# Optimization experiments

Hardware: AMD Instinct MI355X
Metric: run time of the kernel (lower is better)

The kernel has to match this reference:

```python
import jax, jax.numpy as jnp
import numpy as np

MARGIN = 0.3
BIG = 9999999.0


def setup_inputs() -> dict:
    key = jax.random.key(0)
    k1, k2, k3 = jax.random.split(key, 3)
    N, D, D2, NUM_IDS = 8192, 1024, 512, 512
    emb = jax.random.normal(k1, (N, D), dtype=jnp.float32)
    clot_feats_s = jax.random.normal(k2, (N, D2), dtype=jnp.float32)
    label = jax.random.randint(k3, (N,), 0, NUM_IDS, dtype=jnp.int64)
    return {"emb": emb, "label": label, "clot_feats_s": clot_feats_s}


def _margin_ranking_loss(x1, x2, y, margin):
    # torch MarginRankingLoss: mean(max(0, -y*(x1-x2)+margin))
    return jnp.mean(jnp.maximum(0.0, -y * (x1 - x2) + margin))


def reference(emb, label, clot_feats_s):
    N = emb.shape[0]
    # euclidean_dist(emb, emb): [N,N]
    sq = jnp.sum(emb * emb, axis=1)
    dist = sq[:, None] + sq[None, :] - 2.0 * (emb @ emb.T)
    dist = jnp.sqrt(jnp.clip(dist, 1e-12, None))
    # cosine similarity of clot_feats_s with itself: [N,N]
    nrm = jnp.sqrt(jnp.sum(clot_feats_s * clot_feats_s, axis=1))
    cos = (clot_feats_s @ clot_feats_s.T) / (nrm[:, None] * nrm[None, :])
    # same-identity mask
    sim = (label[:, None] == label[None, :]).astype(dist.dtype)
    # batch-hard: top-2 positives (largest masked distance), hardest negative (smallest)
    pos_vals, pos_idx = jax.lax.top_k(dist - BIG * (1.0 - sim), 2)
    dist_ap1, dist_ap2 = pos_vals[:, 0], pos_vals[:, 1]
    neg_mat = dist + BIG * sim
    hard_n_idx = jnp.argmin(neg_mat, axis=1)
    dist_an = jnp.min(neg_mat, axis=1)
    rows = jnp.arange(N)
    # per-row gathers into cosine-sim matrix (detached in original)
    alpha1 = jax.lax.stop_gradient(cos[rows, pos_idx[:, 0]])
    alpha2 = jax.lax.stop_gradient(cos[rows, pos_idx[:, 1]])
    # (alphan gathered in original but unused in the loss)
    y11 = jnp.where(alpha1 < alpha2, -1.0, 1.0)
    y11_m = jnp.where(alpha1 == alpha2, 0.0, 1.0)
    loss11 = _margin_ranking_loss(
        dist_ap2 * y11_m,
        dist_ap1 * y11_m + MARGIN * (alpha1 - alpha2 - y11),
        y11, MARGIN)
    dist_ap1_m = dist_ap1 + MARGIN * (alpha1 - 1.0)
    loss13 = _margin_ranking_loss(dist_an, dist_ap1_m, 1.0, MARGIN)
    loss = 0.1 * loss11 + loss13
    prec = jnp.mean((dist_an > dist_ap1_m).astype(jnp.float32))
    return loss, prec
```

## Files before the change

kernel.cpp:

```cpp
#include <hip/hip_runtime.h>
#include <stdint.h>

#define NR 8192
#define DE 1024
#define DC 512
#define BIGF 9999999.0f
#define MARG 0.3f
#define NEGI -3.0e38f
#define POSI 3.0e38f

typedef __attribute__((ext_vector_type(8))) short bf16x8;
typedef __attribute__((ext_vector_type(4))) float f32x4;

typedef __attribute__((address_space(3))) unsigned int lds_u32;
typedef const __attribute__((address_space(1))) unsigned int glb_u32;

static __device__ __forceinline__ void ld_g2l16(const void* g, void* l) {
    __builtin_amdgcn_global_load_lds((glb_u32*)g, (lds_u32*)l, 16, 0, 0);
}

static __device__ __forceinline__ unsigned short f2bf(float x) {
    unsigned u = __float_as_uint(x);
    unsigned r = u + 0x7FFFu + ((u >> 16) & 1u);
    return (unsigned short)(r >> 16);
}

static __device__ __forceinline__ float b2f(short u) {
    return __uint_as_float(((unsigned)(unsigned short)u) << 16);
}

__global__ __launch_bounds__(256) void k_prep_emb(const float* __restrict__ emb,
                                                  const int* __restrict__ label,
                                                  short* __restrict__ embb,
                                                  float* __restrict__ sq,
                                                  int* __restrict__ cnt) {
    int row = blockIdx.x, tid = threadIdx.x;
    float4 v = ((const float4*)(emb + (size_t)row * DE))[tid];
    float s = v.x * v.x + v.y * v.y + v.z * v.z + v.w * v.w;
    ushort4 b;
    b.x = f2bf(v.x); b.y = f2bf(v.y); b.z = f2bf(v.z); b.w = f2bf(v.w);
    *(ushort4*)&embb[(size_t)row * DE + tid * 4] = b;
    for (int m = 1; m < 64; m <<= 1) s += __shfl_xor(s, m);
    __shared__ float red[4];
    if ((tid & 63) == 0) red[tid >> 6] = s;
    __syncthreads();
    if (tid == 0) {
        sq[row] = red[0] + red[1] + red[2] + red[3];
        atomicAdd(&cnt[label[row]], 1);
    }
}

__global__ __launch_bounds__(256) void k_fill(const int* __restrict__ cnt,
                                              const int* __restrict__ label,
                                              int* __restrict__ clsOff,
                                              int* __restrict__ fill,
                                              int* __restrict__ list) {
    __shared__ int s[512];
    int t = threadIdx.x;
    s[t] = cnt[t];
    s[t + 256] = cnt[t + 256];
    __syncthreads();
    for (int d = 1; d < 512; d <<= 1) {
        int v0 = (t >= d) ? s[t - d] : 0;
        int v1 = s[t + 256 - d];
        __syncthreads();
        s[t] += v0;
        s[t + 256] += v1;
        __syncthreads();
    }
    if (blockIdx.x == 0) {
        clsOff[t] = s[t] - cnt[t];
        clsOff[t + 256] = s[t + 256] - cnt[t + 256];
    }
    int i = blockIdx.x * 256 + t;
    int l = label[i];
    int p = atomicAdd(&fill[l], 1);
    list[s[l] - cnt[l] + p] = i;
}

__global__ __launch_bounds__(256, 3) void k_main(const short* __restrict__ embb,
                                                 const float* __restrict__ sq,
                                                 const int* __restrict__ label,
                                                 unsigned* __restrict__ mnA) {
    const int b = blockIdx.x;
    int r = (int)((129.0f - sqrtf(16641.0f - 8.0f * (float)b)) * 0.5f);
    if (r < 0) r = 0;
    if (r > 63) r = 63;
    while (r > 0 && 64 * r - (r * (r - 1)) / 2 > b) --r;
    while (64 * (r + 1) - ((r + 1) * r) / 2 <= b) ++r;
    const int c = r + (b - (64 * r - (r * (r - 1)) / 2));
    const int i0 = r * 128, j0 = c * 128;

    __shared__ __align__(16) short As[128 * 64];
    __shared__ __align__(16) short Bs[128 * 64];

    const int tid = threadIdx.x;
    const int lane = tid & 63;
    const int w = tid >> 6;
    const int wr = w >> 1, wc = w & 1;
    const int q = lane >> 4, l15 = lane & 15;

    const int g = (tid & 7) ^ ((tid >> 3) & 7);
    const short* gA = embb + (size_t)(i0 + (tid >> 3)) * DE + g * 8;
    const short* gB = embb + (size_t)(j0 + (tid >> 3)) * DE + g * 8;

    const int swz = l15 & 7;

    auto stage = [&](int koff) {
#pragma unroll
        for (int n = 0; n < 4; ++n) {
            ld_g2l16(gA + (size_t)n * 32 * DE + koff, &As[n * 2048 + tid * 8]);
            ld_g2l16(gB + (size_t)n * 32 * DE + koff, &Bs[n * 2048 + tid * 8]);
        }
    };

    stage(0);

    f32x4 acc[4][4];
#pragma unroll
    for (int mi = 0; mi < 4; ++mi)
#pragma unroll
        for (int ni = 0; ni < 4; ++ni) acc[mi][ni] = (f32x4){0.f, 0.f, 0.f, 0.f};

    for (int ks = 0; ks < 16; ++ks) {
        __syncthreads();
        bf16x8 af[2][4], bfr[2][4];
#pragma unroll
        for (int kk = 0; kk < 2; ++kk) {
            const int kc = ((kk * 4 + q) ^ swz) * 8;
#pragma unroll
            for (int mi = 0; mi < 4; ++mi)
                af[kk][mi] = *(const bf16x8*)&As[(wr * 64 + mi * 16 + l15) * 64 + kc];
#pragma unroll
            for (int ni = 0; ni < 4; ++ni)
                bfr[kk][ni] = *(const bf16x8*)&Bs[(wc * 64 + ni * 16 + l15) * 64 + kc];
        }
#pragma unroll
        for (int kk = 0; kk < 2; ++kk)
#pragma unroll
            for (int mi = 0; mi < 4; ++mi)
#pragma unroll
                for (int ni = 0; ni < 4; ++ni)
                    acc[mi][ni] = __builtin_amdgcn_mfma_f32_16x16x32_bf16(af[kk][mi], bfr[kk][ni], acc[mi][ni], 0, 0, 0);
        __syncthreads();
        if (ks < 15) stage((ks + 1) * 64);
    }

    const int rb = i0 + wr * 64, cb = j0 + wc * 64;
    float sqj[4]; int lbj[4]; float cmn[4];
#pragma unroll
    for (int ni = 0; ni < 4; ++ni) {
        int cg = cb + ni * 16 + l15;
        sqj[ni] = sq[cg]; lbj[ni] = label[cg]; cmn[ni] = POSI;
    }
#pragma unroll
    for (int mi = 0; mi < 4; ++mi) {
        float rm[4] = {POSI, POSI, POSI, POSI};
        float sqi[4]; int lbi[4];
#pragma unroll
        for (int rr = 0; rr < 4; ++rr) {
            int rg = rb + mi * 16 + q * 4 + rr;
            sqi[rr] = sq[rg]; lbi[rr] = label[rg];
        }
#pragma unroll
        for (int ni = 0; ni < 4; ++ni)
#pragma unroll
            for (int rr = 0; rr < 4; ++rr) {
                float d2 = fmaf(-2.0f, acc[mi][ni][rr], sqi[rr] + sqj[ni]);
                d2 = fmaxf(d2, 1e-12f);
                float dn = (lbi[rr] == lbj[ni]) ? POSI : d2;
                rm[rr] = fminf(rm[rr], dn);
                cmn[ni] = fminf(cmn[ni], dn);
            }
#pragma unroll
        for (int rr = 0; rr < 4; ++rr) {
            float v = rm[rr];
            v = fminf(v, __shfl_xor(v, 1));
            v = fminf(v, __shfl_xor(v, 2));
            v = fminf(v, __shfl_xor(v, 4));
            v = fminf(v, __shfl_xor(v, 8));
            if (l15 == 0) atomicMin(&mnA[rb + mi * 16 + q * 4 + rr], __float_as_uint(v));
        }
    }
#pragma unroll
    for (int ni = 0; ni < 4; ++ni) {
        float v = cmn[ni];
        v = fminf(v, __shfl_xor(v, 16));
        v = fminf(v, __shfl_xor(v, 32));
        if (q == 0) atomicMin(&mnA[cb + ni * 16 + l15], __float_as_uint(v));
    }
}

__global__ __launch_bounds__(256) void k_pos(const short* __restrict__ embb,
                                             const float* __restrict__ sq,
                                             const float* __restrict__ clot,
                                             const int* __restrict__ label,
                                             const int* __restrict__ cnt,
                                             const int* __restrict__ clsOff,
                                             const int* __restrict__ clsList,
                                             const unsigned* __restrict__ mnA,
                                             float* __restrict__ ap1, float* __restrict__ ap2,
                                             float* __restrict__ an,
                                             float* __restrict__ alpha1, float* __restrict__ alpha2) {
    int wid = threadIdx.x >> 6, lane = threadIdx.x & 63;
    int row = blockIdx.x * 4 + wid;
    int lb = label[row];
    int cc = cnt[lb], off = clsOff[lb];
    float sqiv = sq[row];

    const bf16x8* rp = (const bf16x8*)(embb + (size_t)row * DE + lane * 16);
    bf16x8 ra = rp[0], rb = rp[1];
    float rf[16];
#pragma unroll
    for (int t = 0; t < 8; ++t) { rf[t] = b2f(ra[t]); rf[8 + t] = b2f(rb[t]); }

    float v1 = NEGI, v2 = NEGI;
    int i1 = 0, i2 = 0;

    auto upd = [&](float d2, int j) {
        bool t1 = (d2 > v1) || (d2 == v1 && j < i1);
        bool t2 = (d2 > v2) || (d2 == v2 && j < i2);
        v2 = t1 ? v1 : (t2 ? d2 : v2);
        i2 = t1 ? i1 : (t2 ? j : i2);
        v1 = t1 ? d2 : v1;
        i1 = t1 ? j : i1;
    };

    int m = 0;
    for (; m + 2 <= cc; m += 2) {
        int ja = clsList[off + m], jb = clsList[off + m + 1];
        const bf16x8* pa = (const bf16x8*)(embb + (size_t)ja * DE + lane * 16);
        const bf16x8* pb = (const bf16x8*)(embb + (size_t)jb * DE + lane * 16);
        bf16x8 a0 = pa[0], a1v = pa[1];
        bf16x8 b0 = pb[0], b1v = pb[1];
        float sa = 0.f, sb = 0.f;
#pragma unroll
        for (int t = 0; t < 8; ++t) { sa = fmaf(rf[t], b2f(a0[t]), sa); sb = fmaf(rf[t], b2f(b0[t]), sb); }
#pragma unroll
        for (int t = 0; t < 8; ++t) { sa = fmaf(rf[8 + t], b2f(a1v[t]), sa); sb = fmaf(rf[8 + t], b2f(b1v[t]), sb); }
        for (int mm = 1; mm < 64; mm <<= 1) { sa += __shfl_xor(sa, mm); sb += __shfl_xor(sb, mm); }
        float d2a = fmaxf(fmaf(-2.0f, sa, sqiv + sq[ja]), 1e-12f);
        float d2b = fmaxf(fmaf(-2.0f, sb, sqiv + sq[jb]), 1e-12f);
        if (ja == row) d2a = 1e-12f;
        if (jb == row) d2b = 1e-12f;
        upd(d2a, ja);
        upd(d2b, jb);
    }
    if (m < cc) {
        int j = clsList[off + m];
        float d2;
        if (j == row) {
            d2 = 1e-12f;
        } else {
            const bf16x8* jp = (const bf16x8*)(embb + (size_t)j * DE + lane * 16);
            bf16x8 ja0 = jp[0], ja1 = jp[1];
            float s = 0.f;
#pragma unroll
            for (int t = 0; t < 8; ++t) s = fmaf(rf[t], b2f(ja0[t]), s);
#pragma unroll
            for (int t = 0; t < 8; ++t) s = fmaf(rf[8 + t], b2f(ja1[t]), s);
            for (int mm = 1; mm < 64; mm <<= 1) s += __shfl_xor(s, mm);
            d2 = fmaxf(fmaf(-2.0f, s, sqiv + sq[j]), 1e-12f);
        }
        upd(d2, j);
    }

    float a1 = sqrtf(v1);
    int j1 = i1;
    float a2v; int j2;
    if (cc >= 2) {
        a2v = sqrtf(v2);
        j2 = i2;
    } else {
        float kv = NEGI; int ki = 0;
        for (int cr = lane; cr < NR; cr += 64) {
            if (label[cr] == lb) continue;
            float s = 0.f;
            const short* crow = embb + (size_t)cr * DE;
            const short* rrow = embb + (size_t)row * DE;
            for (int t = 0; t < DE; ++t) s = fmaf(b2f(rrow[t]), b2f(crow[t]), s);
            float d2c = fmaxf(fmaf(-2.0f, s, sqiv + sq[cr]), 1e-12f);
            bool tk = (d2c > kv) || (d2c == kv && cr < ki);
            kv = tk ? d2c : kv; ki = tk ? cr : ki;
        }
        for (int mm = 1; mm < 64; mm <<= 1) {
            float ov = __shfl_xor(kv, mm); int oi = __shfl_xor(ki, mm);
            bool tk = (ov > kv) || (ov == kv && oi < ki);
            kv = tk ? ov : kv; ki = tk ? oi : ki;
        }
        a2v = sqrtf(kv) - BIGF;
        j2 = ki;
    }

    const float4* c4 = (const float4*)clot;
    float s1 = 0.f, s2 = 0.f, n0 = 0.f, n1 = 0.f, n2 = 0.f;
    for (int t = lane; t < DC / 4; t += 64) {
        float4 a = c4[(size_t)row * (DC / 4) + t];
        float4 b1 = c4[(size_t)j1 * (DC / 4) + t];
        float4 b2 = c4[(size_t)j2 * (DC / 4) + t];
        s1 += a.x * b1.x + a.y * b1.y + a.z * b1.z + a.w * b1.w;
        s2 += a.x * b2.x + a.y * b2.y + a.z * b2.z + a.w * b2.w;
        n0 += a.x * a.x + a.y * a.y + a.z * a.z + a.w * a.w;
        n1 += b1.x * b1.x + b1.y * b1.y + b1.z * b1.z + b1.w * b1.w;
        n2 += b2.x * b2.x + b2.y * b2.y + b2.z * b2.z + b2.w * b2.w;
    }
    for (int mm = 1; mm < 64; mm <<= 1) {
        s1 += __shfl_xor(s1, mm); s2 += __shfl_xor(s2, mm);
        n0 += __shfl_xor(n0, mm); n1 += __shfl_xor(n1, mm); n2 += __shfl_xor(n2, mm);
    }
    if (lane == 0) {
        ap1[row] = a1; ap2[row] = a2v;
        an[row] = sqrtf(__uint_as_float(mnA[row]));
        alpha1[row] = s1 / (sqrtf(n0) * sqrtf(n1));
        alpha2[row] = s2 / (sqrtf(n0) * sqrtf(n2));
    }
}

__global__ __launch_bounds__(256) void k_final(const float* __restrict__ ap1, const float* __restrict__ ap2,
                                               const float* __restrict__ an,
                                               const float* __restrict__ alpha1, const float* __restrict__ alpha2,
                                               float* __restrict__ out) {
    int tid = threadIdx.x;
    float sl11 = 0.f, sl13 = 0.f, sp = 0.f;
    for (int row = tid; row < NR; row += 256) {
        float a1 = alpha1[row], a2 = alpha2[row];
        float dap1 = ap1[row], dap2 = ap2[row], dan = an[row];
        float y = (a1 < a2) ? -1.f : 1.f;
        float ym = (a1 == a2) ? 0.f : 1.f;
        float x1 = dap2 * ym;
        float x2 = dap1 * ym + MARG * (a1 - a2 - y);
        sl11 += fmaxf(0.f, -y * (x1 - x2) + MARG);
        float ap1m = dap1 + MARG * (a1 - 1.f);
        sl13 += fmaxf(0.f, -(dan - ap1m) + MARG);
        sp += (dan > ap1m) ? 1.f : 0.f;
    }
    for (int m = 1; m < 64; m <<= 1) {
        sl11 += __shfl_xor(sl11, m);
        sl13 += __shfl_xor(sl13, m);
        sp += __shfl_xor(sp, m);
    }
    __shared__ float r11[4], r13[4], rp[4];
    if ((tid & 63) == 0) { r11[tid >> 6] = sl11; r13[tid >> 6] = sl13; rp[tid >> 6] = sp; }
    __syncthreads();
    if (tid == 0) {
        float t11 = r11[0] + r11[1] + r11[2] + r11[3];
        float t13 = r13[0] + r13[1] + r13[2] + r13[3];
        float tp = rp[0] + rp[1] + rp[2] + rp[3];
        out[0] = 0.1f * (t11 / (float)NR) + t13 / (float)NR;
        out[1] = tp / (float)NR;
    }
}

extern "C" void kernel_launch(void* const* d_in, const int* in_sizes, int n_in,
                              void* d_out, int out_size, void* d_ws, size_t ws_size,
                              hipStream_t stream) {
    const float* emb = (const float*)d_in[0];
    const int* label = (const int*)d_in[1];
    const float* clot = (const float*)d_in[2];
    float* out = (float*)d_out;

    char* ws = (char*)d_ws;
    size_t off = 0;
    auto alloc = [&](size_t bytes) -> char* {
        char* p = ws + off;
        off = (off + bytes + 255) & ~(size_t)255;
        return p;
    };
    short*    embb = (short*)alloc((size_t)NR * DE * 2);
    float*    sq   = (float*)alloc(NR * 4);
    int*      cnt  = (int*)alloc(512 * 4);
    int*      fill = (int*)alloc(512 * 4);
    int*      cOff = (int*)alloc(512 * 4);
    int*      list = (int*)alloc(NR * 4);
    unsigned* mnA  = (unsigned*)alloc((size_t)NR * 4);
    float*    ap1  = (float*)alloc(NR * 4);
    float*    ap2  = (float*)alloc(NR * 4);
    float*    an   = (float*)alloc(NR * 4);
    float*    al1  = (float*)alloc(NR * 4);
    float*    al2  = (float*)alloc(NR * 4);

    hipMemsetAsync(cnt, 0, 2 * 512 * 4, stream);
    hipMemsetAsync(mnA, 0xFF, (size_t)NR * 4, stream);

    k_prep_emb<<<dim3(NR), dim3(256), 0, stream>>>(emb, label, embb, sq, cnt);
    k_fill<<<dim3(NR / 256), dim3(256), 0, stream>>>(cnt, label, cOff, fill, list);
    k_main<<<dim3(2080), dim3(256), 0, stream>>>(embb, sq, label, mnA);
    k_pos<<<dim3(NR / 4), dim3(256), 0, stream>>>(embb, sq, clot, label, cnt, cOff, list,
                                                  mnA, ap1, ap2, an, al1, al2);
    k_final<<<dim3(1), dim3(256), 0, stream>>>(ap1, ap2, an, al1, al2, out);
}
```

Baseline: 232.7 us.

## Split each row's positive search across four waves and fold mnA init into prep

k_pos now gives each row a whole 256-thread block instead of one wave. The four waves split the same-class candidate list and merge their top-2 results through shared memory. The rare fallback scan is also spread over all 256 threads. Separately, the memset of the min-distance buffer is replaced by a store in k_prep_emb, which removes one memset launch. This adds parallelism to a latency-bound per-row loop, at the cost of more blocks, a block barrier, and three idle waves during the cosine stage.

```diff
diff --git a/kernel.cpp b/kernel.cpp
--- a/kernel.cpp
+++ b/kernel.cpp
@@ -33,7 +33,8 @@
                                                   const int* __restrict__ label,
                                                   short* __restrict__ embb,
                                                   float* __restrict__ sq,
-                                                  int* __restrict__ cnt) {
+                                                  int* __restrict__ cnt,
+                                                  unsigned* __restrict__ mnA) {
     int row = blockIdx.x, tid = threadIdx.x;
     float4 v = ((const float4*)(emb + (size_t)row * DE))[tid];
     float s = v.x * v.x + v.y * v.y + v.z * v.z + v.w * v.w;
@@ -47,6 +48,7 @@
     if (tid == 0) {
         sq[row] = red[0] + red[1] + red[2] + red[3];
         atomicAdd(&cnt[label[row]], 1);
+        mnA[row] = 0xFFFFFFFFu;
     }
 }
 
@@ -202,11 +204,11 @@
                                              float* __restrict__ ap1, float* __restrict__ ap2,
                                              float* __restrict__ an,
                                              float* __restrict__ alpha1, float* __restrict__ alpha2) {
-    int wid = threadIdx.x >> 6, lane = threadIdx.x & 63;
-    int row = blockIdx.x * 4 + wid;
-    int lb = label[row];
-    int cc = cnt[lb], off = clsOff[lb];
-    float sqiv = sq[row];
+    const int row = blockIdx.x;
+    const int tid = threadIdx.x, wid = tid >> 6, lane = tid & 63;
+    const int lb = label[row];
+    const int cc = cnt[lb], off = clsOff[lb];
+    const float sqiv = sq[row];
 
     const bf16x8* rp = (const bf16x8*)(embb + (size_t)row * DE + lane * 16);
     bf16x8 ra = rp[0], rb = rp[1];
@@ -216,7 +218,6 @@
 
     float v1 = NEGI, v2 = NEGI;
     int i1 = 0, i2 = 0;
-
     auto upd = [&](float d2, int j) {
         bool t1 = (d2 > v1) || (d2 == v1 && j < i1);
         bool t2 = (d2 > v2) || (d2 == v2 && j < i2);
@@ -226,54 +227,52 @@
         i1 = t1 ? j : i1;
     };
 
-    int m = 0;
-    for (; m + 2 <= cc; m += 2) {
-        int ja = clsList[off + m], jb = clsList[off + m + 1];
-        const bf16x8* pa = (const bf16x8*)(embb + (size_t)ja * DE + lane * 16);
-        const bf16x8* pb = (const bf16x8*)(embb + (size_t)jb * DE + lane * 16);
-        bf16x8 a0 = pa[0], a1v = pa[1];
-        bf16x8 b0 = pb[0], b1v = pb[1];
-        float sa = 0.f, sb = 0.f;
-#pragma unroll
-        for (int t = 0; t < 8; ++t) { sa = fmaf(rf[t], b2f(a0[t]), sa); sb = fmaf(rf[t], b2f(b0[t]), sb); }
-#pragma unroll
-        for (int t = 0; t < 8; ++t) { sa = fmaf(rf[8 + t], b2f(a1v[t]), sa); sb = fmaf(rf[8 + t], b2f(b1v[t]), sb); }
-        for (int mm = 1; mm < 64; mm <<= 1) { sa += __shfl_xor(sa, mm); sb += __shfl_xor(sb, mm); }
-        float d2a = fmaxf(fmaf(-2.0f, sa, sqiv + sq[ja]), 1e-12f);
-        float d2b = fmaxf(fmaf(-2.0f, sb, sqiv + sq[jb]), 1e-12f);
-        if (ja == row) d2a = 1e-12f;
-        if (jb == row) d2b = 1e-12f;
-        upd(d2a, ja);
-        upd(d2b, jb);
-    }
-    if (m < cc) {
+    for (int m = wid; m < cc; m += 4) {
         int j = clsList[off + m];
         float d2;
         if (j == row) {
             d2 = 1e-12f;
         } else {
             const bf16x8* jp = (const bf16x8*)(embb + (size_t)j * DE + lane * 16);
-            bf16x8 ja0 = jp[0], ja1 = jp[1];
+            bf16x8 ja = jp[0], jb = jp[1];
             float s = 0.f;
 #pragma unroll
-            for (int t = 0; t < 8; ++t) s = fmaf(rf[t], b2f(ja0[t]), s);
-#pragma unroll
-            for (int t = 0; t < 8; ++t) s = fmaf(rf[8 + t], b2f(ja1[t]), s);
+            for (int t = 0; t < 8; ++t) s = fmaf(rf[t], b2f(ja[t]), s);
+#pragma unroll
+            for (int t = 0; t < 8; ++t) s = fmaf(rf[8 + t], b2f(jb[t]), s);
             for (int mm = 1; mm < 64; mm <<= 1) s += __shfl_xor(s, mm);
             d2 = fmaxf(fmaf(-2.0f, s, sqiv + sq[j]), 1e-12f);
         }
         upd(d2, j);
     }
 
-    float a1 = sqrtf(v1);
-    int j1 = i1;
+    __shared__ float mv1[4], mv2[4];
+    __shared__ int mi1[4], mi2[4];
+    if (lane == 0) { mv1[wid] = v1; mi1[wid] = i1; mv2[wid] = v2; mi2[wid] = i2; }
+    __syncthreads();
+    float V1 = NEGI, V2 = NEGI;
+    int I1 = 0, I2 = 0;
+#pragma unroll
+    for (int k = 0; k < 8; ++k) {
+        float d2 = (k < 4) ? mv1[k] : mv2[k - 4];
+        int j = (k < 4) ? mi1[k] : mi2[k - 4];
+        bool t1 = (d2 > V1) || (d2 == V1 && j < I1);
+        bool t2 = (d2 > V2) || (d2 == V2 && j < I2);
+        V2 = t1 ? V1 : (t2 ? d2 : V2);
+        I2 = t1 ? I1 : (t2 ? j : I2);
+        V1 = t1 ? d2 : V1;
+        I1 = t1 ? j : I1;
+    }
+
+    float a1 = sqrtf(V1);
+    int j1 = I1;
     float a2v; int j2;
     if (cc >= 2) {
-        a2v = sqrtf(v2);
-        j2 = i2;
+        a2v = sqrtf(V2);
+        j2 = I2;
     } else {
         float kv = NEGI; int ki = 0;
-        for (int cr = lane; cr < NR; cr += 64) {
+        for (int cr = tid; cr < NR; cr += 256) {
             if (label[cr] == lb) continue;
             float s = 0.f;
             const short* crow = embb + (size_t)cr * DE;
@@ -288,31 +287,42 @@
             bool tk = (ov > kv) || (ov == kv && oi < ki);
             kv = tk ? ov : kv; ki = tk ? oi : ki;
         }
+        __shared__ float fkv[4]; __shared__ int fki[4];
+        if (lane == 0) { fkv[wid] = kv; fki[wid] = ki; }
+        __syncthreads();
+        kv = fkv[0]; ki = fki[0];
+#pragma unroll
+        for (int k = 1; k < 4; ++k) {
+            bool tk = (fkv[k] > kv) || (fkv[k] == kv && fki[k] < ki);
+            kv = tk ? fkv[k] : kv; ki = tk ? fki[k] : ki;
+        }
         a2v = sqrtf(kv) - BIGF;
         j2 = ki;
     }
 
-    const float4* c4 = (const float4*)clot;
-    float s1 = 0.f, s2 = 0.f, n0 = 0.f, n1 = 0.f, n2 = 0.f;
-    for (int t = lane; t < DC / 4; t += 64) {
-        float4 a = c4[(size_t)row * (DC / 4) + t];
-        float4 b1 = c4[(size_t)j1 * (DC / 4) + t];
-        float4 b2 = c4[(size_t)j2 * (DC / 4) + t];
-        s1 += a.x * b1.x + a.y * b1.y + a.z * b1.z + a.w * b1.w;
-        s2 += a.x * b2.x + a.y * b2.y + a.z * b2.z + a.w * b2.w;
-        n0 += a.x * a.x + a.y * a.y + a.z * a.z + a.w * a.w;
-        n1 += b1.x * b1.x + b1.y * b1.y + b1.z * b1.z + b1.w * b1.w;
-        n2 += b2.x * b2.x + b2.y * b2.y + b2.z * b2.z + b2.w * b2.w;
-    }
-    for (int mm = 1; mm < 64; mm <<= 1) {
-        s1 += __shfl_xor(s1, mm); s2 += __shfl_xor(s2, mm);
-        n0 += __shfl_xor(n0, mm); n1 += __shfl_xor(n1, mm); n2 += __shfl_xor(n2, mm);
-    }
-    if (lane == 0) {
-        ap1[row] = a1; ap2[row] = a2v;
-        an[row] = sqrtf(__uint_as_float(mnA[row]));
-        alpha1[row] = s1 / (sqrtf(n0) * sqrtf(n1));
-        alpha2[row] = s2 / (sqrtf(n0) * sqrtf(n2));
+    if (wid == 0) {
+        const float4* c4 = (const float4*)clot;
+        float s1 = 0.f, s2 = 0.f, n0 = 0.f, n1 = 0.f, n2 = 0.f;
+        for (int t = lane; t < DC / 4; t += 64) {
+            float4 a = c4[(size_t)row * (DC / 4) + t];
+            float4 b1 = c4[(size_t)j1 * (DC / 4) + t];
+            float4 b2 = c4[(size_t)j2 * (DC / 4) + t];
+            s1 += a.x * b1.x + a.y * b1.y + a.z * b1.z + a.w * b1.w;
+            s2 += a.x * b2.x + a.y * b2.y + a.z * b2.z + a.w * b2.w;
+            n0 += a.x * a.x + a.y * a.y + a.z * a.z + a.w * a.w;
+            n1 += b1.x * b1.x + b1.y * b1.y + b1.z * b1.z + b1.w * b1.w;
+            n2 += b2.x * b2.x + b2.y * b2.y + b2.z * b2.z + b2.w * b2.w;
+        }
+        for (int mm = 1; mm < 64; mm <<= 1) {
+            s1 += __shfl_xor(s1, mm); s2 += __shfl_xor(s2, mm);
+            n0 += __shfl_xor(n0, mm); n1 += __shfl_xor(n1, mm); n2 += __shfl_xor(n2, mm);
+        }
+        if (lane == 0) {
+            ap1[row] = a1; ap2[row] = a2v;
+            an[row] = sqrtf(__uint_as_float(mnA[row]));
+            alpha1[row] = s1 / (sqrtf(n0) * sqrtf(n1));
+            alpha2[row] = s2 / (sqrtf(n0) * sqrtf(n2));
+        }
     }
 }
 
@@ -380,12 +390,11 @@
     float*    al2  = (float*)alloc(NR * 4);
 
     hipMemsetAsync(cnt, 0, 2 * 512 * 4, stream);
-    hipMemsetAsync(mnA, 0xFF, (size_t)NR * 4, stream);
-
-    k_prep_emb<<<dim3(NR), dim3(256), 0, stream>>>(emb, label, embb, sq, cnt);
+
+    k_prep_emb<<<dim3(NR), dim3(256), 0, stream>>>(emb, label, embb, sq, cnt, mnA);
     k_fill<<<dim3(NR / 256), dim3(256), 0, stream>>>(cnt, label, cOff, fill, list);
     k_main<<<dim3(2080), dim3(256), 0, stream>>>(embb, sq, label, mnA);
-    k_pos<<<dim3(NR / 4), dim3(256), 0, stream>>>(embb, sq, clot, label, cnt, cOff, list,
-                                                  mnA, ap1, ap2, an, al1, al2);
+    k_pos<<<dim3(NR), dim3(256), 0, stream>>>(embb, sq, clot, label, cnt, cOff, list,
+                                              mnA, ap1, ap2, an, al1, al2);
     k_final<<<dim3(1), dim3(256), 0, stream>>>(ap1, ap2, an, al1, al2, out);
 }
```

Measured after the change: 238.5 us. 1.02x slower.

## Cache same-class distances from GEMM epilogue to skip recomputation in positive pass

Applied to the files above, without the earlier changes.

The main Gram-matrix kernel now writes every same-label squared distance into a per-class 64x64 buffer, indexed by each row's position within its class. The positive-mining kernel then reads these cached values with one lane per class member and a wave-wide top-2 reduction, instead of recomputing bf16 dot products for every class member. Classes larger than the cap fall back to the old dot-product path. The prep kernel also handles four rows per block without LDS and initialises the min array itself, which removes one memset. In exchange, the epilogue gains scattered global stores and mIdx loads, and the code depends on the fallback for classes above 64 members.

```diff
diff --git a/kernel.cpp b/kernel.cpp
--- a/kernel.cpp
+++ b/kernel.cpp
@@ -8,6 +8,7 @@
 #define MARG 0.3f
 #define NEGI -3.0e38f
 #define POSI 3.0e38f
+#define CAP 64
 
 typedef __attribute__((ext_vector_type(8))) short bf16x8;
 typedef __attribute__((ext_vector_type(4))) float f32x4;
@@ -33,20 +34,26 @@
                                                   const int* __restrict__ label,
                                                   short* __restrict__ embb,
                                                   float* __restrict__ sq,
-                                                  int* __restrict__ cnt) {
-    int row = blockIdx.x, tid = threadIdx.x;
-    float4 v = ((const float4*)(emb + (size_t)row * DE))[tid];
-    float s = v.x * v.x + v.y * v.y + v.z * v.z + v.w * v.w;
-    ushort4 b;
-    b.x = f2bf(v.x); b.y = f2bf(v.y); b.z = f2bf(v.z); b.w = f2bf(v.w);
-    *(ushort4*)&embb[(size_t)row * DE + tid * 4] = b;
+                                                  int* __restrict__ cnt,
+                                                  unsigned* __restrict__ mnA) {
+    int w = threadIdx.x >> 6, lane = threadIdx.x & 63;
+    int row = blockIdx.x * 4 + w;
+    const float4* src = (const float4*)(emb + (size_t)row * DE);
+    ushort4* dst = (ushort4*)(embb + (size_t)row * DE);
+    float s = 0.f;
+#pragma unroll
+    for (int c = 0; c < 4; ++c) {
+        float4 v = src[c * 64 + lane];
+        s += v.x * v.x + v.y * v.y + v.z * v.z + v.w * v.w;
+        ushort4 b;
+        b.x = f2bf(v.x); b.y = f2bf(v.y); b.z = f2bf(v.z); b.w = f2bf(v.w);
+        dst[c * 64 + lane] = b;
+    }
     for (int m = 1; m < 64; m <<= 1) s += __shfl_xor(s, m);
-    __shared__ float red[4];
-    if ((tid & 63) == 0) red[tid >> 6] = s;
-    __syncthreads();
-    if (tid == 0) {
-        sq[row] = red[0] + red[1] + red[2] + red[3];
+    if (lane == 0) {
+        sq[row] = s;
         atomicAdd(&cnt[label[row]], 1);
+        mnA[row] = 0xFFFFFFFFu;
     }
 }
 
@@ -54,7 +61,8 @@
                                               const int* __restrict__ label,
                                               int* __restrict__ clsOff,
                                               int* __restrict__ fill,
-                                              int* __restrict__ list) {
+                                              int* __restrict__ list,
+                                              int* __restrict__ mIdx) {
     __shared__ int s[512];
     int t = threadIdx.x;
     s[t] = cnt[t];
@@ -76,12 +84,15 @@
     int l = label[i];
     int p = atomicAdd(&fill[l], 1);
     list[s[l] - cnt[l] + p] = i;
+    mIdx[i] = p;
 }
 
 __global__ __launch_bounds__(256, 3) void k_main(const short* __restrict__ embb,
                                                  const float* __restrict__ sq,
                                                  const int* __restrict__ label,
-                                                 unsigned* __restrict__ mnA) {
+                                                 const int* __restrict__ mIdx,
+                                                 unsigned* __restrict__ mnA,
+                                                 float* __restrict__ posmat) {
     const int b = blockIdx.x;
     int r = (int)((129.0f - sqrtf(16641.0f - 8.0f * (float)b)) * 0.5f);
     if (r < 0) r = 0;
@@ -168,6 +179,16 @@
             for (int rr = 0; rr < 4; ++rr) {
                 float d2 = fmaf(-2.0f, acc[mi][ni][rr], sqi[rr] + sqj[ni]);
                 d2 = fmaxf(d2, 1e-12f);
+                if (lbi[rr] == lbj[ni]) {
+                    int gi = rb + mi * 16 + q * 4 + rr;
+                    int gj = cb + ni * 16 + l15;
+                    int a = mIdx[gi], bb = mIdx[gj];
+                    if (a < CAP && bb < CAP) {
+                        float* pm = posmat + (size_t)lbi[rr] * CAP * CAP;
+                        pm[a * CAP + bb] = d2;
+                        pm[bb * CAP + a] = d2;
+                    }
+                }
                 float dn = (lbi[rr] == lbj[ni]) ? POSI : d2;
                 rm[rr] = fminf(rm[rr], dn);
                 cmn[ni] = fminf(cmn[ni], dn);
@@ -198,6 +219,8 @@
                                              const int* __restrict__ cnt,
                                              const int* __restrict__ clsOff,
                                              const int* __restrict__ clsList,
+                                             const int* __restrict__ mIdx,
+                                             const float* __restrict__ posmat,
                                              const unsigned* __restrict__ mnA,
                                              float* __restrict__ ap1, float* __restrict__ ap2,
                                              float* __restrict__ an,
@@ -208,15 +231,8 @@
     int cc = cnt[lb], off = clsOff[lb];
     float sqiv = sq[row];
 
-    const bf16x8* rp = (const bf16x8*)(embb + (size_t)row * DE + lane * 16);
-    bf16x8 ra = rp[0], rb = rp[1];
-    float rf[16];
-#pragma unroll
-    for (int t = 0; t < 8; ++t) { rf[t] = b2f(ra[t]); rf[8 + t] = b2f(rb[t]); }
-
     float v1 = NEGI, v2 = NEGI;
     int i1 = 0, i2 = 0;
-
     auto upd = [&](float d2, int j) {
         bool t1 = (d2 > v1) || (d2 == v1 && j < i1);
         bool t2 = (d2 > v2) || (d2 == v2 && j < i2);
@@ -226,43 +242,43 @@
         i1 = t1 ? j : i1;
     };
 
-    int m = 0;
-    for (; m + 2 <= cc; m += 2) {
-        int ja = clsList[off + m], jb = clsList[off + m + 1];
-        const bf16x8* pa = (const bf16x8*)(embb + (size_t)ja * DE + lane * 16);
-        const bf16x8* pb = (const bf16x8*)(embb + (size_t)jb * DE + lane * 16);
-        bf16x8 a0 = pa[0], a1v = pa[1];
-        bf16x8 b0 = pb[0], b1v = pb[1];
-        float sa = 0.f, sb = 0.f;
-#pragma unroll
-        for (int t = 0; t < 8; ++t) { sa = fmaf(rf[t], b2f(a0[t]), sa); sb = fmaf(rf[t], b2f(b0[t]), sb); }
-#pragma unroll
-        for (int t = 0; t < 8; ++t) { sa = fmaf(rf[8 + t], b2f(a1v[t]), sa); sb = fmaf(rf[8 + t], b2f(b1v[t]), sb); }
-        for (int mm = 1; mm < 64; mm <<= 1) { sa += __shfl_xor(sa, mm); sb += __shfl_xor(sb, mm); }
-        float d2a = fmaxf(fmaf(-2.0f, sa, sqiv + sq[ja]), 1e-12f);
-        float d2b = fmaxf(fmaf(-2.0f, sb, sqiv + sq[jb]), 1e-12f);
-        if (ja == row) d2a = 1e-12f;
-        if (jb == row) d2b = 1e-12f;
-        upd(d2a, ja);
-        upd(d2b, jb);
-    }
-    if (m < cc) {
-        int j = clsList[off + m];
-        float d2;
-        if (j == row) {
-            d2 = 1e-12f;
-        } else {
-            const bf16x8* jp = (const bf16x8*)(embb + (size_t)j * DE + lane * 16);
-            bf16x8 ja0 = jp[0], ja1 = jp[1];
-            float s = 0.f;
-#pragma unroll
-            for (int t = 0; t < 8; ++t) s = fmaf(rf[t], b2f(ja0[t]), s);
-#pragma unroll
-            for (int t = 0; t < 8; ++t) s = fmaf(rf[8 + t], b2f(ja1[t]), s);
-            for (int mm = 1; mm < 64; mm <<= 1) s += __shfl_xor(s, mm);
-            d2 = fmaxf(fmaf(-2.0f, s, sqiv + sq[j]), 1e-12f);
-        }
-        upd(d2, j);
+    if (cc <= CAP) {
+        const int self = mIdx[row];
+        if (lane < cc) {
+            float d2 = (lane == self) ? 1e-12f
+                                      : posmat[((size_t)lb * CAP + self) * CAP + lane];
+            upd(d2, clsList[off + lane]);
+        }
+        for (int d = 1; d < 64; d <<= 1) {
+            float o1 = __shfl_xor(v1, d), o2 = __shfl_xor(v2, d);
+            int oi1 = __shfl_xor(i1, d), oi2 = __shfl_xor(i2, d);
+            upd(o1, oi1);
+            upd(o2, oi2);
+        }
+    } else {
+        const bf16x8* rp = (const bf16x8*)(embb + (size_t)row * DE + lane * 16);
+        bf16x8 ra = rp[0], rb = rp[1];
+        float rf[16];
+#pragma unroll
+        for (int t = 0; t < 8; ++t) { rf[t] = b2f(ra[t]); rf[8 + t] = b2f(rb[t]); }
+        for (int m = 0; m < cc; ++m) {
+            int j = clsList[off + m];
+            float d2;
+            if (j == row) {
+                d2 = 1e-12f;
+            } else {
+                const bf16x8* jp = (const bf16x8*)(embb + (size_t)j * DE + lane * 16);
+                bf16x8 ja = jp[0], jb = jp[1];
+                float s = 0.f;
+#pragma unroll
+                for (int t = 0; t < 8; ++t) s = fmaf(rf[t], b2f(ja[t]), s);
+#pragma unroll
+                for (int t = 0; t < 8; ++t) s = fmaf(rf[8 + t], b2f(jb[t]), s);
+                for (int mm = 1; mm < 64; mm <<= 1) s += __shfl_xor(s, mm);
+                d2 = fmaxf(fmaf(-2.0f, s, sqiv + sq[j]), 1e-12f);
+            }
+            upd(d2, j);
+        }
     }
 
     float a1 = sqrtf(v1);
@@ -367,11 +383,13 @@
         return p;
     };
     short*    embb = (short*)alloc((size_t)NR * DE * 2);
+    float*    pmat = (float*)alloc((size_t)512 * CAP * CAP * 4);
     float*    sq   = (float*)alloc(NR * 4);
     int*      cnt  = (int*)alloc(512 * 4);
     int*      fill = (int*)alloc(512 * 4);
     int*      cOff = (int*)alloc(512 * 4);
     int*      list = (int*)alloc(NR * 4);
+    int*      mIdx = (int*)alloc(NR * 4);
     unsigned* mnA  = (unsigned*)alloc((size_t)NR * 4);
     float*    ap1  = (float*)alloc(NR * 4);
     float*    ap2  = (float*)alloc(NR * 4);
@@ -380,12 +398,11 @@
     float*    al2  = (float*)alloc(NR * 4);
 
     hipMemsetAsync(cnt, 0, 2 * 512 * 4, stream);
-    hipMemsetAsync(mnA, 0xFF, (size_t)NR * 4, stream);
-
-    k_prep_emb<<<dim3(NR), dim3(256), 0, stream>>>(emb, label, embb, sq, cnt);
-    k_fill<<<dim3(NR / 256), dim3(256), 0, stream>>>(cnt, label, cOff, fill, list);
-    k_main<<<dim3(2080), dim3(256), 0, stream>>>(embb, sq, label, mnA);
+
+    k_prep_emb<<<dim3(NR / 4), dim3(256), 0, stream>>>(emb, label, embb, sq, cnt, mnA);
+    k_fill<<<dim3(NR / 256), dim3(256), 0, stream>>>(cnt, label, cOff, fill, list, mIdx);
+    k_main<<<dim3(2080), dim3(256), 0, stream>>>(embb, sq, label, mIdx, mnA, pmat);
     k_pos<<<dim3(NR / 4), dim3(256), 0, stream>>>(embb, sq, clot, label, cnt, cOff, list,
-                                                  mnA, ap1, ap2, an, al1, al2);
+                                                  mIdx, pmat, mnA, ap1, ap2, an, al1, al2);
     k_final<<<dim3(1), dim3(256), 0, stream>>>(ap1, ap2, an, al1, al2, out);
 }
```

New measurement: 219.1 us. 1.06x faster.
